# Kernel tuning notes

Measured on AMD Instinct MI355X. Metric: run time of the kernel, lower is better.

Reference implementation:

```python
import jax, jax.numpy as jnp
import numpy as np

C = 256
NUM_HEADS = 4
HEAD_DIM = C // NUM_HEADS
GROUPS = 32
EPS = 1e-5


def setup_inputs() -> dict:
    key = jax.random.key(0)
    ks = jax.random.split(key, 7)
    B, H, W = 4, 64, 64
    x = jax.random.normal(ks[0], (B, C, H, W), dtype=jnp.float32)
    gn_w = jax.random.normal(ks[1], (C,), dtype=jnp.float32) * 0.02 + 1.0
    gn_b = jax.random.normal(ks[2], (C,), dtype=jnp.float32) * 0.02
    qkv_w = jax.random.normal(ks[3], (3 * C, C), dtype=jnp.float32) * (1.0 / np.sqrt(C))
    qkv_b = jax.random.normal(ks[4], (3 * C,), dtype=jnp.float32) * 0.02
    out_w = jax.random.normal(ks[5], (C, C), dtype=jnp.float32) * (1.0 / np.sqrt(C))
    out_b = jax.random.normal(ks[6], (C,), dtype=jnp.float32) * 0.02
    return {"x": x, "gn_w": gn_w, "gn_b": gn_b, "qkv_w": qkv_w,
            "qkv_b": qkv_b, "out_w": out_w, "out_b": out_b}


def _group_norm(x, w, b):
    # x: [B, C, H, W]; normalize over (C/GROUPS, H, W) per group
    B, Cc, Hh, Ww = x.shape
    xg = x.reshape(B, GROUPS, Cc // GROUPS, Hh, Ww)
    mean = jnp.mean(xg, axis=(2, 3, 4), keepdims=True)
    var = jnp.var(xg, axis=(2, 3, 4), keepdims=True)
    xg = (xg - mean) * jax.lax.rsqrt(var + EPS)
    xn = xg.reshape(B, Cc, Hh, Ww)
    return xn * w[None, :, None, None] + b[None, :, None, None]


def reference(x, gn_w, gn_b, qkv_w, qkv_b, out_w, out_b):
    B, Cc, Hh, Ww = x.shape
    N = Hh * Ww
    h = _group_norm(x, gn_w, gn_b).reshape(B, Cc, N)
    # qkv conv1d (kernel size 1) == pointwise linear over channel dim
    qkv = jnp.einsum('oc,bcn->bon', qkv_w, h) + qkv_b[None, :, None]
    q, k, v = jnp.split(qkv, 3, axis=1)
    q = q.reshape(B, NUM_HEADS, HEAD_DIM, N)
    k = k.reshape(B, NUM_HEADS, HEAD_DIM, N)
    v = v.reshape(B, NUM_HEADS, HEAD_DIM, N)
    scale = 1.0 / np.sqrt(HEAD_DIM)
    attn = jnp.einsum('bhdk,bhdl->bhkl', q, k) * scale  # [B, H, N, N]
    attn = jax.nn.softmax(attn, axis=-1)
    out = jnp.einsum('bhkl,bhdl->bhdk', attn, v)  # [B, H, D, N]
    out = out.reshape(B, Cc, N)
    out = jnp.einsum('oc,bcn->bon', out_w, out) + out_b[None, :, None]
    return x + out.reshape(B, Cc, Hh, Ww)
```

## Files before the change

### kernel.cpp

```cpp
#include <hip/hip_runtime.h>
#include <cstdint>

typedef __bf16 bf16_t;
typedef __bf16 bf16x4 __attribute__((ext_vector_type(4)));
typedef __bf16 bf16x8 __attribute__((ext_vector_type(8)));
typedef float f32x4 __attribute__((ext_vector_type(4)));
typedef unsigned int u32x2 __attribute__((ext_vector_type(2)));
typedef unsigned int u32x4 __attribute__((ext_vector_type(4)));

#define B_ 4
#define C_ 256
#define N_ 4096
#define NH_ 4
#define HD_ 64

static __device__ __forceinline__ f32x4 mfma_bf16(bf16x8 a, bf16x8 b, f32x4 c) {
  return __builtin_amdgcn_mfma_f32_16x16x32_bf16(a, b, c, 0, 0, 0);
}

static __device__ __forceinline__ void async16(const void* g, void* l) {
  __builtin_amdgcn_global_load_lds(
      (__attribute__((address_space(1))) void*)(uintptr_t)g,
      (__attribute__((address_space(3))) void*)(uint32_t)(uintptr_t)l,
      16, 0, 0);
}

static __device__ __forceinline__ float fexp2(float x) {
#if __has_builtin(__builtin_amdgcn_exp2f)
  return __builtin_amdgcn_exp2f(x);
#else
  return exp2f(x);
#endif
}

static __device__ __forceinline__ unsigned pack_bf16(float lo, float hi) {
  bf16x4 t;
  t[0] = (bf16_t)lo;
  t[1] = (bf16_t)hi;
  return *(unsigned*)&t;
}

__global__ __launch_bounds__(256) void k_pre(const float* __restrict__ x,
                                             const float* __restrict__ gn_w,
                                             const float* __restrict__ gn_b,
                                             const float* __restrict__ qkv_w,
                                             const float* __restrict__ out_w,
                                             float* __restrict__ gnscale,
                                             float* __restrict__ gnshift,
                                             bf16_t* __restrict__ w1,
                                             bf16_t* __restrict__ w2) {
  __shared__ float red_s[4], red_ss[4];
  if (blockIdx.x >= 128) {
    int i = (blockIdx.x - 128) * 256 + threadIdx.x;
    if (i < 3 * C_ * C_) w1[i] = (bf16_t)qkv_w[i];
    else w2[i - 3 * C_ * C_] = (bf16_t)out_w[i - 3 * C_ * C_];
    return;
  }
  const int bg = blockIdx.x;
  const int b = bg >> 5, g = bg & 31;
  const float4* p4 = (const float4*)(x + (size_t)(b * C_ + g * 8) * N_);
  float s = 0.f, ss = 0.f;
  for (int i = threadIdx.x; i < 8192; i += 256) {
    float4 v = p4[i];
    s += (v.x + v.y) + (v.z + v.w);
    ss += (v.x * v.x + v.y * v.y) + (v.z * v.z + v.w * v.w);
  }
  for (int off = 32; off > 0; off >>= 1) {
    s += __shfl_down(s, off);
    ss += __shfl_down(ss, off);
  }
  const int wid = threadIdx.x >> 6, lane = threadIdx.x & 63;
  if (lane == 0) { red_s[wid] = s; red_ss[wid] = ss; }
  __syncthreads();
  if (threadIdx.x < 8) {
    float S = (red_s[0] + red_s[1]) + (red_s[2] + red_s[3]);
    float SS = (red_ss[0] + red_ss[1]) + (red_ss[2] + red_ss[3]);
    float mean = S * (1.f / 32768.f);
    float var = SS * (1.f / 32768.f) - mean * mean;
    float rstd = rsqrtf(var + 1e-5f);
    int c = g * 8 + threadIdx.x;
    float w = gn_w[c];
    gnscale[b * C_ + c] = w * rstd;
    gnshift[b * C_ + c] = gn_b[c] - mean * rstd * w;
  }
}

__global__ __launch_bounds__(256) void k_gn_apply(const float* __restrict__ x,
                                                  const float* __restrict__ gnscale,
                                                  const float* __restrict__ gnshift,
                                                  bf16_t* __restrict__ h) {
  __shared__ bf16_t T[32 * 258];
  const int t = threadIdx.x;
  const int tok0 = blockIdx.x * 32;
  const int b = tok0 >> 12;
  const int n0 = tok0 & (N_ - 1);
  const int nl = t & 31, cset = t >> 5;
  const float* xb = x + ((size_t)(b * C_ + cset * 32) << 12) + n0 + nl;
  const float* scp = gnscale + b * C_ + cset * 32;
  const float* shp = gnshift + b * C_ + cset * 32;
#pragma unroll
  for (int j = 0; j < 32; ++j) {
    float y = xb[(size_t)j << 12] * scp[j] + shp[j];
    T[nl * 258 + cset * 32 + j] = (bf16_t)y;
  }
  __syncthreads();
  const int c4 = t & 63;
#pragma unroll
  for (int p = 0; p < 8; ++p) {
    const int tokl = p * 4 + (t >> 6);
    const int idx = tokl * 258 + c4 * 4;
    uint2 v;
    v.x = *(const unsigned*)&T[idx];
    v.y = *(const unsigned*)&T[idx + 2];
    *(uint2*)(h + ((size_t)(tok0 + tokl) << 8) + c4 * 4) = v;
  }
}

__global__ __launch_bounds__(256) void k_gemm_qkv(const bf16_t* __restrict__ h,
                                                  const bf16_t* __restrict__ w1,
                                                  const float* __restrict__ qkv_b,
                                                  bf16_t* __restrict__ Qb,
                                                  bf16_t* __restrict__ Kb,
                                                  bf16_t* __restrict__ Vb) {
  __shared__ bf16_t As[128 * 32], Bs[128 * 32];
  const int tid = threadIdx.x, lane = tid & 63, wid = tid >> 6;
  const int g = lane >> 4, q = lane & 15;
  const int wm = wid >> 1, wn = wid & 1;
  const int m0 = blockIdx.x * 128;
  const int o0 = blockIdx.y * 128;
  f32x4 acc[4][4] = {};
  const int srow = lane >> 2, scol = (lane & 3) * 8;
  for (int kc = 0; kc < 8; ++kc) {
    const int k0 = kc * 32;
#pragma unroll
    for (int j = 0; j < 2; ++j) {
      const int chunk = wid + j * 4;
      async16(h + (size_t)(m0 + chunk * 16 + srow) * C_ + k0 + scol, &As[chunk * 512]);
      async16(w1 + (size_t)(o0 + chunk * 16 + srow) * C_ + k0 + scol, &Bs[chunk * 512]);
    }
    __syncthreads();
    bf16x8 a[4], bb[4];
#pragma unroll
    for (int t = 0; t < 4; ++t) {
      a[t] = *(const bf16x8*)&As[(wm * 64 + t * 16 + q) * 32 + g * 8];
      bb[t] = *(const bf16x8*)&Bs[(wn * 64 + t * 16 + q) * 32 + g * 8];
    }
#pragma unroll
    for (int mi = 0; mi < 4; ++mi)
#pragma unroll
      for (int ni = 0; ni < 4; ++ni)
        acc[mi][ni] = mfma_bf16(a[mi], bb[ni], acc[mi][ni]);
    __syncthreads();
  }
  const float QSCALE = 0.1803368801111244f;
#pragma unroll
  for (int ni = 0; ni < 4; ++ni) {
    const int o = o0 + wn * 64 + ni * 16 + q;
    const float bias = qkv_b[o];
    const int mat = o >> 8;
    const int c = o & 255, hh = c >> 6, d = c & 63;
#pragma unroll
    for (int mi = 0; mi < 4; ++mi) {
      const int tokb = m0 + wm * 64 + mi * 16 + g * 4;
      const int b = tokb >> 12, n = tokb & (N_ - 1);
      const size_t bh = (size_t)(b * NH_ + hh);
      f32x4 t = acc[mi][ni] + bias;
      if (mat == 0) {
#pragma unroll
        for (int r = 0; r < 4; ++r)
          Qb[(bh * N_ + n + r) * HD_ + d] = (bf16_t)(t[r] * QSCALE);
      } else if (mat == 1) {
#pragma unroll
        for (int r = 0; r < 4; ++r)
          Kb[(bh * N_ + n + r) * HD_ + d] = (bf16_t)t[r];
      } else {
        *(bf16x4*)(Vb + (bh * HD_ + d) * N_ + n) = __builtin_convertvector(t, bf16x4);
      }
    }
  }
}

__global__ __launch_bounds__(512) void k_attn(const bf16_t* __restrict__ Qb,
                                              const bf16_t* __restrict__ Kb,
                                              const bf16_t* __restrict__ Vb,
                                              bf16_t* __restrict__ op0,
                                              bf16_t* __restrict__ op1,
                                              float* __restrict__ lsum) {
  __shared__ __align__(16) bf16_t Ks[2][4096];
  __shared__ __align__(16) bf16_t Vs[2][4096];
  const int tid = threadIdx.x, lane = tid & 63, wid = tid >> 6;
  const int g = lane >> 4, q = lane & 15;
  const int qs = q & 7;
  int bid = blockIdx.x;
  bid = (bid & 7) * 64 + (bid >> 3);
  const int kh = bid & 1;
  const int qt = (bid >> 1) & 15;
  const int bh = bid >> 5;
  const int nq0 = qt * 256 + wid * 32;
  const int k00 = kh * (N_ / 2);
  const int NT = (N_ / 2) / 64;
  const size_t base = (size_t)bh << 18;
  const bf16_t* Qp = Qb + base;
  const bf16_t* Kp = Kb + base;
  const bf16_t* Vp = Vb + base;

  const bf16x8 bqA0 = *(const bf16x8*)(Qp + (size_t)(nq0 + q) * HD_ + g * 8);
  const bf16x8 bqA1 = *(const bf16x8*)(Qp + (size_t)(nq0 + q) * HD_ + 32 + g * 8);
  const bf16x8 bqB0 = *(const bf16x8*)(Qp + (size_t)(nq0 + 16 + q) * HD_ + g * 8);
  const bf16x8 bqB1 = *(const bf16x8*)(Qp + (size_t)(nq0 + 16 + q) * HD_ + 32 + g * 8);

  const int srow = lane >> 3;
  const int sc16 = (lane & 7) ^ srow;

  f32x4 laccA = {}, laccB = {};
  f32x4 accA[4] = {}, accB[4] = {};
  bf16x8 ones;
#pragma unroll
  for (int i = 0; i < 8; ++i) ones[i] = (bf16_t)1.0f;

  async16(Kp + (size_t)(k00 + wid * 8 + srow) * HD_ + sc16 * 8, &Ks[0][wid * 512]);
  async16(Vp + (size_t)(wid * 8 + srow) * N_ + k00 + sc16 * 8, &Vs[0][wid * 512]);
  __syncthreads();

  const bf16_t* kS = Kp + (size_t)(k00 + 64 + wid * 8 + srow) * HD_ + sc16 * 8;
  const bf16_t* vS = Vp + (size_t)(wid * 8 + srow) * N_ + k00 + 64 + sc16 * 8;

  for (int t = 0; t < NT; ++t) {
    const int buf = t & 1;
    if (t < NT - 1) {
      async16(kS, &Ks[buf ^ 1][wid * 512]);
      async16(vS, &Vs[buf ^ 1][wid * 512]);
      kS += 64 * HD_;
      vS += 64;
    }
    const bf16_t* Kl = Ks[buf];
    const bf16_t* Vl = Vs[buf];
    f32x4 z = {0.f, 0.f, 0.f, 0.f};
    f32x4 sA[4], sB[4];
#pragma unroll
    for (int kb = 0; kb < 4; ++kb) {
      bf16x8 k0 = *(const bf16x8*)(Kl + (kb * 16 + q) * 64 + ((g ^ qs) * 8));
      bf16x8 k1 = *(const bf16x8*)(Kl + (kb * 16 + q) * 64 + (((4 + g) ^ qs) * 8));
      sA[kb] = mfma_bf16(k0, bqA0, z);
      sB[kb] = mfma_bf16(k0, bqB0, z);
      sA[kb] = mfma_bf16(k1, bqA1, sA[kb]);
      sB[kb] = mfma_bf16(k1, bqB1, sB[kb]);
    }
#pragma unroll
    for (int kb = 0; kb < 4; ++kb)
#pragma unroll
      for (int r = 0; r < 4; ++r) {
        sA[kb][r] = fexp2(sA[kb][r]);
        sB[kb][r] = fexp2(sB[kb][r]);
      }
    bf16x8 pbA[2], pbB[2];
#pragma unroll
    for (int s = 0; s < 2; ++s) {
      const f32x4* st = s ? sB : sA;
      bf16x8* pb = s ? pbB : pbA;
#pragma unroll
      for (int h = 0; h < 2; ++h) {
        unsigned u0 = pack_bf16(st[2 * h][0], st[2 * h][1]);
        unsigned u1 = pack_bf16(st[2 * h][2], st[2 * h][3]);
        unsigned u2 = pack_bf16(st[2 * h + 1][0], st[2 * h + 1][1]);
        unsigned u3 = pack_bf16(st[2 * h + 1][2], st[2 * h + 1][3]);
        u32x4 w;
#if __has_builtin(__builtin_amdgcn_permlane32_swap) && __has_builtin(__builtin_amdgcn_permlane16_swap)
        u32x2 a02 = __builtin_amdgcn_permlane32_swap(u0, u2, false, false);
        u32x2 r02 = __builtin_amdgcn_permlane16_swap(a02[0], a02[1], false, false);
        u32x2 a13 = __builtin_amdgcn_permlane32_swap(u1, u3, false, false);
        u32x2 r13 = __builtin_amdgcn_permlane16_swap(a13[0], a13[1], false, false);
        w[0] = r02[0]; w[2] = r02[1]; w[1] = r13[0]; w[3] = r13[1];
#else
        const int sl0 = (g & 1) * 32 + q, sl1 = sl0 + 16;
        w[0] = (g < 2) ? __shfl((int)u0, sl0) : __shfl((int)u2, sl0);
        w[1] = (g < 2) ? __shfl((int)u1, sl0) : __shfl((int)u3, sl0);
        w[2] = (g < 2) ? __shfl((int)u0, sl1) : __shfl((int)u2, sl1);
        w[3] = (g < 2) ? __shfl((int)u1, sl1) : __shfl((int)u3, sl1);
#endif
        pb[h] = *(bf16x8*)&w;
      }
    }
    laccA = mfma_bf16(ones, pbA[0], laccA);
    laccA = mfma_bf16(ones, pbA[1], laccA);
    laccB = mfma_bf16(ones, pbB[0], laccB);
    laccB = mfma_bf16(ones, pbB[1], laccB);
#pragma unroll
    for (int db = 0; db < 4; ++db) {
      bf16x8 v0 = *(const bf16x8*)(Vl + (db * 16 + q) * 64 + ((g ^ qs) * 8));
      bf16x8 v1 = *(const bf16x8*)(Vl + (db * 16 + q) * 64 + (((4 + g) ^ qs) * 8));
      accA[db] = mfma_bf16(v0, pbA[0], accA[db]);
      accB[db] = mfma_bf16(v0, pbB[0], accB[db]);
      accA[db] = mfma_bf16(v1, pbA[1], accA[db]);
      accB[db] = mfma_bf16(v1, pbB[1], accB[db]);
    }
    __syncthreads();
  }

  bf16_t* Op = (kh == 0 ? op0 : op1) + (size_t)bh * N_ * HD_;
  bf16_t* opA = Op + (size_t)(nq0 + q) * HD_;
  bf16_t* opB = opA + 16 * HD_;
#pragma unroll
  for (int db = 0; db < 4; ++db) {
    *(bf16x4*)(opA + db * 16 + g * 4) = __builtin_convertvector(accA[db], bf16x4);
    *(bf16x4*)(opB + db * 16 + g * 4) = __builtin_convertvector(accB[db], bf16x4);
  }
  if (g == 0) {
    const size_t mlb = (size_t)(kh * 16 + bh) * N_;
    lsum[mlb + nq0 + q] = laccA[0];
    lsum[mlb + nq0 + 16 + q] = laccB[0];
  }
}

__global__ __launch_bounds__(256) void k_attn_combine(const bf16_t* __restrict__ op0,
                                                      const bf16_t* __restrict__ op1,
                                                      const float* __restrict__ lsum,
                                                      bf16_t* __restrict__ att) {
  const int gid = blockIdx.x * 256 + threadIdx.x;
  const int d8 = gid & 7;
  const int q = (gid >> 3) & (N_ - 1);
  const int bh = gid >> 15;
  const size_t ro = ((size_t)bh * N_ + q) * HD_ + d8 * 8;
  const float l = lsum[(size_t)bh * N_ + q] + lsum[(size_t)(16 + bh) * N_ + q];
  const float inv = 1.0f / l;
  const bf16x8 o0 = *(const bf16x8*)(op0 + ro);
  const bf16x8 o1 = *(const bf16x8*)(op1 + ro);
  bf16x8 r;
#pragma unroll
  for (int j = 0; j < 8; ++j)
    r[j] = (bf16_t)(((float)o0[j] + (float)o1[j]) * inv);
  const int b = bh >> 2, hh = bh & 3;
  *(bf16x8*)(att + ((size_t)b * N_ + q) * C_ + hh * HD_ + d8 * 8) = r;
}

__global__ __launch_bounds__(256) void k_gemm_out(const bf16_t* __restrict__ att,
                                                  const bf16_t* __restrict__ w2,
                                                  const float* __restrict__ out_b,
                                                  const float* __restrict__ x,
                                                  float* __restrict__ out) {
  __shared__ bf16_t As[128 * 32], Bs[128 * 32];
  const int tid = threadIdx.x, lane = tid & 63, wid = tid >> 6;
  const int g = lane >> 4, q = lane & 15;
  const int wm = wid >> 1, wn = wid & 1;
  const int m0 = blockIdx.x * 128;
  const int o0 = blockIdx.y * 128;
  f32x4 acc[4][4] = {};
  const int srow = lane >> 2, scol = (lane & 3) * 8;
  for (int kc = 0; kc < 8; ++kc) {
    const int k0 = kc * 32;
#pragma unroll
    for (int j = 0; j < 2; ++j) {
      const int chunk = wid + j * 4;
      async16(att + (size_t)(m0 + chunk * 16 + srow) * C_ + k0 + scol, &As[chunk * 512]);
      async16(w2 + (size_t)(o0 + chunk * 16 + srow) * C_ + k0 + scol, &Bs[chunk * 512]);
    }
    __syncthreads();
    bf16x8 a[4], bb[4];
#pragma unroll
    for (int t = 0; t < 4; ++t) {
      a[t] = *(const bf16x8*)&As[(wm * 64 + t * 16 + q) * 32 + g * 8];
      bb[t] = *(const bf16x8*)&Bs[(wn * 64 + t * 16 + q) * 32 + g * 8];
    }
#pragma unroll
    for (int mi = 0; mi < 4; ++mi)
#pragma unroll
      for (int ni = 0; ni < 4; ++ni)
        acc[mi][ni] = mfma_bf16(a[mi], bb[ni], acc[mi][ni]);
    __syncthreads();
  }
#pragma unroll
  for (int ni = 0; ni < 4; ++ni) {
    const int o = o0 + wn * 64 + ni * 16 + q;
    const float bias = out_b[o];
#pragma unroll
    for (int mi = 0; mi < 4; ++mi) {
      const int tokb = m0 + wm * 64 + mi * 16 + g * 4;
      const int b = tokb >> 12, n = tokb & (N_ - 1);
      const size_t idx = ((size_t)(b * C_ + o) << 12) + n;
      const float4 xv = *(const float4*)(x + idx);
      f32x4 t = acc[mi][ni];
      float4 r = make_float4(t[0] + bias + xv.x, t[1] + bias + xv.y,
                             t[2] + bias + xv.z, t[3] + bias + xv.w);
      *(float4*)(out + idx) = r;
    }
  }
}

extern "C" void kernel_launch(void* const* d_in, const int* in_sizes, int n_in,
                              void* d_out, int out_size, void* d_ws, size_t ws_size,
                              hipStream_t stream) {
  (void)in_sizes; (void)n_in; (void)out_size; (void)ws_size;
  const float* x = (const float*)d_in[0];
  const float* gn_w = (const float*)d_in[1];
  const float* gn_b = (const float*)d_in[2];
  const float* qkv_w = (const float*)d_in[3];
  const float* qkv_b = (const float*)d_in[4];
  const float* out_w = (const float*)d_in[5];
  const float* out_b = (const float*)d_in[6];
  float* out = (float*)d_out;

  char* ws = (char*)d_ws;
  float* gnscale = (float*)ws;
  float* gnshift = gnscale + 1024;
  bf16_t* w1bf = (bf16_t*)(ws + 8192);
  bf16_t* w2bf = w1bf + 196608;
  bf16_t* hbuf = w2bf + 65536;
  bf16_t* Qb = hbuf + 4194304;
  bf16_t* Kb = Qb + 4194304;
  bf16_t* Vb = Kb + 4194304;
  bf16_t* op1 = Vb + 4194304;
  float* lsum = (float*)(op1 + 4194304);

  k_pre<<<1152, 256, 0, stream>>>(x, gn_w, gn_b, qkv_w, out_w, gnscale, gnshift, w1bf, w2bf);
  k_gn_apply<<<512, 256, 0, stream>>>(x, gnscale, gnshift, hbuf);
  k_gemm_qkv<<<dim3(128, 6), 256, 0, stream>>>(hbuf, w1bf, qkv_b, Qb, Kb, Vb);
  k_attn<<<512, 512, 0, stream>>>(Qb, Kb, Vb, hbuf, op1, lsum);
  k_attn_combine<<<2048, 256, 0, stream>>>(hbuf, op1, lsum, Qb);
  k_gemm_out<<<dim3(128, 2), 256, 0, stream>>>(Qb, w2bf, out_b, x, out);
}
```

Baseline: 121.7 us.

## Fuse attention split-combine into output GEMM and add MFMA priority hints

Removes the separate combine kernel. The output projection GEMM now reads both partial attention outputs, sums them and scales by the reciprocal softmax denominator while filling its shared-memory A tile. This avoids a launch and a full intermediate write and read, but replaces async global-to-LDS loads with synchronous register loads and duplicates the combine across the two output-column blocks. The attention kernel also raises wave priority around its MFMA sections to favor matrix-core issue.

```diff
diff --git a/kernel.cpp b/kernel.cpp
--- a/kernel.cpp
+++ b/kernel.cpp
@@ -237,6 +237,7 @@
     const bf16_t* Vl = Vs[buf];
     f32x4 z = {0.f, 0.f, 0.f, 0.f};
     f32x4 sA[4], sB[4];
+    __builtin_amdgcn_s_setprio(1);
 #pragma unroll
     for (int kb = 0; kb < 4; ++kb) {
       bf16x8 k0 = *(const bf16x8*)(Kl + (kb * 16 + q) * 64 + ((g ^ qs) * 8));
@@ -246,6 +247,7 @@
       sA[kb] = mfma_bf16(k1, bqA1, sA[kb]);
       sB[kb] = mfma_bf16(k1, bqB1, sB[kb]);
     }
+    __builtin_amdgcn_s_setprio(0);
 #pragma unroll
     for (int kb = 0; kb < 4; ++kb)
 #pragma unroll
@@ -281,6 +283,7 @@
         pb[h] = *(bf16x8*)&w;
       }
     }
+    __builtin_amdgcn_s_setprio(1);
     laccA = mfma_bf16(ones, pbA[0], laccA);
     laccA = mfma_bf16(ones, pbA[1], laccA);
     laccB = mfma_bf16(ones, pbB[0], laccB);
@@ -294,6 +297,7 @@
       accA[db] = mfma_bf16(v1, pbA[1], accA[db]);
       accB[db] = mfma_bf16(v1, pbB[1], accB[db]);
     }
+    __builtin_amdgcn_s_setprio(0);
     __syncthreads();
   }
 
@@ -312,47 +316,59 @@
   }
 }
 
-__global__ __launch_bounds__(256) void k_attn_combine(const bf16_t* __restrict__ op0,
-                                                      const bf16_t* __restrict__ op1,
-                                                      const float* __restrict__ lsum,
-                                                      bf16_t* __restrict__ att) {
-  const int gid = blockIdx.x * 256 + threadIdx.x;
-  const int d8 = gid & 7;
-  const int q = (gid >> 3) & (N_ - 1);
-  const int bh = gid >> 15;
-  const size_t ro = ((size_t)bh * N_ + q) * HD_ + d8 * 8;
-  const float l = lsum[(size_t)bh * N_ + q] + lsum[(size_t)(16 + bh) * N_ + q];
-  const float inv = 1.0f / l;
-  const bf16x8 o0 = *(const bf16x8*)(op0 + ro);
-  const bf16x8 o1 = *(const bf16x8*)(op1 + ro);
-  bf16x8 r;
-#pragma unroll
-  for (int j = 0; j < 8; ++j)
-    r[j] = (bf16_t)(((float)o0[j] + (float)o1[j]) * inv);
-  const int b = bh >> 2, hh = bh & 3;
-  *(bf16x8*)(att + ((size_t)b * N_ + q) * C_ + hh * HD_ + d8 * 8) = r;
-}
-
-__global__ __launch_bounds__(256) void k_gemm_out(const bf16_t* __restrict__ att,
+__global__ __launch_bounds__(256) void k_gemm_out(const bf16_t* __restrict__ op0,
+                                                  const bf16_t* __restrict__ op1,
+                                                  const float* __restrict__ lsum,
                                                   const bf16_t* __restrict__ w2,
                                                   const float* __restrict__ out_b,
                                                   const float* __restrict__ x,
                                                   float* __restrict__ out) {
   __shared__ bf16_t As[128 * 32], Bs[128 * 32];
+  __shared__ float invl[4 * 128];
   const int tid = threadIdx.x, lane = tid & 63, wid = tid >> 6;
   const int g = lane >> 4, q = lane & 15;
   const int wm = wid >> 1, wn = wid & 1;
   const int m0 = blockIdx.x * 128;
-  const int o0 = blockIdx.y * 128;
+  const int o0c = blockIdx.y * 128;
+  const int srow = lane >> 2, scol = (lane & 3) * 8;
+
+#pragma unroll
+  for (int ii = 0; ii < 2; ++ii) {
+    const int idx = tid + ii * 256;
+    const int hh = idx >> 7, tokl = idx & 127;
+    const int tok = m0 + tokl;
+    const int b = tok >> 12, n = tok & (N_ - 1);
+    const int bh = b * NH_ + hh;
+    const float l = lsum[(size_t)bh * N_ + n] + lsum[(size_t)(16 + bh) * N_ + n];
+    invl[idx] = 1.0f / l;
+  }
+  __syncthreads();
+
+  const int tokl_s = (wid & 3) * 16 + srow;
+  (void)tokl_s;
+
   f32x4 acc[4][4] = {};
-  const int srow = lane >> 2, scol = (lane & 3) * 8;
   for (int kc = 0; kc < 8; ++kc) {
     const int k0 = kc * 32;
+    const int hh = k0 >> 6;
+    const int d = (k0 & 63) + scol;
 #pragma unroll
     for (int j = 0; j < 2; ++j) {
       const int chunk = wid + j * 4;
-      async16(att + (size_t)(m0 + chunk * 16 + srow) * C_ + k0 + scol, &As[chunk * 512]);
-      async16(w2 + (size_t)(o0 + chunk * 16 + srow) * C_ + k0 + scol, &Bs[chunk * 512]);
+      const int tokl = chunk * 16 + srow;
+      const int tok = m0 + tokl;
+      const int b = tok >> 12, n = tok & (N_ - 1);
+      const size_t ro = ((size_t)(b * NH_ + hh) * N_ + n) * HD_ + d;
+      const bf16x8 a0 = *(const bf16x8*)(op0 + ro);
+      const bf16x8 a1 = *(const bf16x8*)(op1 + ro);
+      const float il = invl[hh * 128 + tokl];
+      u32x4 wpk;
+#pragma unroll
+      for (int p = 0; p < 4; ++p)
+        wpk[p] = pack_bf16(((float)a0[2 * p] + (float)a1[2 * p]) * il,
+                           ((float)a0[2 * p + 1] + (float)a1[2 * p + 1]) * il);
+      *(u32x4*)&As[chunk * 512 + srow * 32 + scol] = wpk;
+      async16(w2 + (size_t)(o0c + chunk * 16 + srow) * C_ + k0 + scol, &Bs[chunk * 512]);
     }
     __syncthreads();
     bf16x8 a[4], bb[4];
@@ -370,7 +386,7 @@
   }
 #pragma unroll
   for (int ni = 0; ni < 4; ++ni) {
-    const int o = o0 + wn * 64 + ni * 16 + q;
+    const int o = o0c + wn * 64 + ni * 16 + q;
     const float bias = out_b[o];
 #pragma unroll
     for (int mi = 0; mi < 4; ++mi) {
@@ -415,6 +431,5 @@
   k_gn_apply<<<512, 256, 0, stream>>>(x, gnscale, gnshift, hbuf);
   k_gemm_qkv<<<dim3(128, 6), 256, 0, stream>>>(hbuf, w1bf, qkv_b, Qb, Kb, Vb);
   k_attn<<<512, 512, 0, stream>>>(Qb, Kb, Vb, hbuf, op1, lsum);
-  k_attn_combine<<<2048, 256, 0, stream>>>(hbuf, op1, lsum, Qb);
-  k_gemm_out<<<dim3(128, 2), 256, 0, stream>>>(Qb, w2bf, out_b, x, out);
-}
+  k_gemm_out<<<dim3(128, 2), 256, 0, stream>>>(hbuf, op1, lsum, w2bf, out_b, x, out);
+}
```

Result: no change. 120.3 us (-1.2%).
